# Kernel optimization log

Measured on AMD Instinct MI355X. Metric: run time of the kernel, lower is better.

The kernel has to match this reference:

```python
import jax, jax.numpy as jnp
import numpy as np

# shapes
B, S, D, V = 2, 2048, 1024, 32000
C = 8            # n_cycles
P = 256          # actual planes = min(n_planes_init, D // 2)
EPS = 1.1920929e-07  # torch RMSNorm default eps for float32 (finfo.eps)


def _rmsnorm(x, w):
    ms = jnp.mean(x * x, axis=-1, keepdims=True)
    return x * jax.lax.rsqrt(ms + EPS) * w


def setup_inputs() -> dict:
    key = jax.random.key(0)
    ks = jax.random.split(key, 10)
    tokens = jax.random.randint(ks[0], (B, S), 0, V, dtype=jnp.int32)
    embed_weight = jax.random.normal(ks[1], (V, D), dtype=jnp.float32) * 0.02
    lm_head_weight = jax.random.normal(ks[2], (V, D), dtype=jnp.float32) * 0.02
    out_norm_weight = jnp.ones((D,), dtype=jnp.float32)
    # per-cycle learned params (non-trivial values for numerics)
    angles = jax.random.normal(ks[3], (C, P), dtype=jnp.float32) * 0.1
    scales = 1.0 + jax.random.normal(ks[4], (C, D), dtype=jnp.float32) * 0.01
    shifts = jax.random.normal(ks[5], (C, D), dtype=jnp.float32) * 0.01
    norm_weights = 1.0 + jax.random.normal(ks[6], (C, D), dtype=jnp.float32) * 0.01
    mix_weight = jnp.array([0.1, 0.8, 0.1], dtype=jnp.float32)
    # plane pairs: per-cycle permutation of D, pi = perm[:P], pj = perm[P:2P]
    pi_list, pj_list = [], []
    for c in range(C):
        perm = jax.random.permutation(jax.random.fold_in(ks[7], c), D)
        pi_list.append(perm[:P])
        pj_list.append(perm[P:2 * P])
    pi_all = jnp.stack(pi_list).astype(jnp.int32)  # [C, P]
    pj_all = jnp.stack(pj_list).astype(jnp.int32)  # [C, P]
    return {
        "tokens": tokens,
        "embed_weight": embed_weight,
        "angles": angles,
        "scales": scales,
        "shifts": shifts,
        "norm_weights": norm_weights,
        "mix_weight": mix_weight,
        "out_norm_weight": out_norm_weight,
        "lm_head_weight": lm_head_weight,
        "pi_all": pi_all,
        "pj_all": pj_all,
    }


def reference(tokens, embed_weight, angles, scales, shifts, norm_weights,
              mix_weight, out_norm_weight, lm_head_weight, pi_all, pj_all):
    x = embed_weight[tokens].astype(jnp.float32)  # [B, S, D]
    n_cycles = angles.shape[0]
    for c in range(n_cycles):
        # temporal mix: shifted-left / self / shifted-right
        left = jnp.pad(x[:, :-1, :], ((0, 0), (1, 0), (0, 0)))
        right = jnp.pad(x[:, 1:, :], ((0, 0), (0, 1), (0, 0)))
        x = mix_weight[0] * left + mix_weight[1] * x + mix_weight[2] * right
        # Givens rotations on disjoint plane pairs (gather -> rotate -> scatter)
        pi, pj = pi_all[c], pj_all[c]
        cos_a = jnp.cos(angles[c])
        sin_a = jnp.sin(angles[c])
        xi = x[..., pi]  # [B, S, P]
        xj = x[..., pj]
        x_new = x.at[..., pi].set(xi * cos_a - xj * sin_a)
        x_new = x_new.at[..., pj].set(xi * sin_a + xj * cos_a)
        # scale/shift + SiLU, then RMSNorm residual update
        x_act = jax.nn.silu(x_new * scales[c] + shifts[c])
        x = x + _rmsnorm(x_act - x, norm_weights[c])
    x = _rmsnorm(x, out_norm_weight)
    return jnp.einsum("bsd,vd->bsv", x, lm_head_weight)  # [B, S, V]
```

## Files before the change

kernel.cpp:

```cpp
#include <hip/hip_runtime.h>

#define B_SZ   2
#define S_LEN  2048
#define D_DIM  1024
#define V_DIM  32000
#define NTOK   (B_SZ * S_LEN)
#define NCYC   8
#define NPLANES 256
#define EPS_F  1.1920929e-07f
#define NTILE  2000

typedef float  f32x4  __attribute__((ext_vector_type(4)));
typedef __bf16 bf16x8 __attribute__((ext_vector_type(8)));

__device__ __forceinline__ unsigned short f32_to_bf16(float f) {
    unsigned int u = __builtin_bit_cast(unsigned int, f);
    u += 0x7fffu + ((u >> 16) & 1u);
    return (unsigned short)(u >> 16);
}

__device__ __forceinline__ float4 mix3(float a, const float4& u, float b,
                                       const float4& v, float c, const float4& w) {
    return make_float4(a * u.x + b * v.x + c * w.x,
                       a * u.y + b * v.y + c * w.y,
                       a * u.z + b * v.z + c * w.z,
                       a * u.w + b * v.w + c * w.w);
}

__global__ __launch_bounds__(256) void k_cyc(
    int c,
    const int* __restrict__ tokens, const float* __restrict__ table,
    const float* __restrict__ xin, float* __restrict__ xout,
    const float* __restrict__ angles, const float* __restrict__ scales,
    const float* __restrict__ shifts, const float* __restrict__ normw,
    const float* __restrict__ mixw, const float* __restrict__ outnw,
    unsigned short* __restrict__ xbf,
    const int* __restrict__ pi, const int* __restrict__ pj,
    const float* __restrict__ lmhead, unsigned short* __restrict__ wbf)
{
    __shared__ float lx[4][D_DIM];
    __shared__ float red[4][4];
    const int b = blockIdx.x, tid = threadIdx.x;
    const int wv = tid >> 6, ln = tid & 63;
    const int t0 = b << 2;
    const int s0 = t0 & (S_LEN - 1);

    float4 row[4];
    float4 hl = make_float4(0.f, 0.f, 0.f, 0.f);
    float4 hr = make_float4(0.f, 0.f, 0.f, 0.f);
    if (c == 0) {
        #pragma unroll
        for (int i = 0; i < 4; ++i) {
            const int tok = tokens[t0 + i];
            row[i] = ((const float4*)(table + (size_t)tok * D_DIM))[tid];
        }
        if (s0 > 0) {
            const int tok = tokens[t0 - 1];
            hl = ((const float4*)(table + (size_t)tok * D_DIM))[tid];
        }
        if (s0 + 4 < S_LEN) {
            const int tok = tokens[t0 + 4];
            hr = ((const float4*)(table + (size_t)tok * D_DIM))[tid];
        }
    } else {
        #pragma unroll
        for (int i = 0; i < 4; ++i)
            row[i] = ((const float4*)(xin + (size_t)(t0 + i) * D_DIM))[tid];
        if (s0 > 0)
            hl = ((const float4*)(xin + (size_t)(t0 - 1) * D_DIM))[tid];
        if (s0 + 4 < S_LEN)
            hr = ((const float4*)(xin + (size_t)(t0 + 4) * D_DIM))[tid];
    }
    const float mw0 = mixw[0], mw1 = mixw[1], mw2 = mixw[2];

    float4 m[4];
    m[0] = mix3(mw0, hl,     mw1, row[0], mw2, row[1]);
    m[1] = mix3(mw0, row[0], mw1, row[1], mw2, row[2]);
    m[2] = mix3(mw0, row[1], mw1, row[2], mw2, row[3]);
    m[3] = mix3(mw0, row[2], mw1, row[3], mw2, hr);
    #pragma unroll
    for (int i = 0; i < 4; ++i) ((float4*)lx[i])[tid] = m[i];
    __syncthreads();

    const int ip = pi[tid], jp = pj[tid];
    float sa, ca;
    sincosf(angles[tid], &sa, &ca);
    float xi[4], xj[4];
    #pragma unroll
    for (int i = 0; i < 4; ++i) { xi[i] = lx[i][ip]; xj[i] = lx[i][jp]; }
    #pragma unroll
    for (int i = 0; i < 4; ++i) {
        lx[i][ip] = xi[i] * ca - xj[i] * sa;
        lx[i][jp] = xi[i] * sa + xj[i] * ca;
    }
    __syncthreads();

    const float4 sc = ((const float4*)scales)[tid];
    const float4 sh = ((const float4*)shifts)[tid];
    const float4 nw = ((const float4*)normw)[tid];
    float4 r[4];
    float sum[4];
    #pragma unroll
    for (int i = 0; i < 4; ++i) {
        const float4 xn = ((const float4*)lx[i])[tid];
        const float a0 = xn.x * sc.x + sh.x;
        const float a1 = xn.y * sc.y + sh.y;
        const float a2 = xn.z * sc.z + sh.z;
        const float a3 = xn.w * sc.w + sh.w;
        r[i].x = a0 / (1.f + expf(-a0)) - m[i].x;
        r[i].y = a1 / (1.f + expf(-a1)) - m[i].y;
        r[i].z = a2 / (1.f + expf(-a2)) - m[i].z;
        r[i].w = a3 / (1.f + expf(-a3)) - m[i].w;
        sum[i] = r[i].x * r[i].x + r[i].y * r[i].y
               + r[i].z * r[i].z + r[i].w * r[i].w;
    }
    #pragma unroll
    for (int off = 32; off > 0; off >>= 1)
        #pragma unroll
        for (int i = 0; i < 4; ++i) sum[i] += __shfl_down(sum[i], off, 64);
    if (ln == 0) {
        red[wv][0] = sum[0]; red[wv][1] = sum[1];
        red[wv][2] = sum[2]; red[wv][3] = sum[3];
    }
    __syncthreads();
    #pragma unroll
    for (int i = 0; i < 4; ++i) {
        const float tot = red[0][i] + red[1][i] + red[2][i] + red[3][i];
        const float inv = rsqrtf(tot * (1.0f / D_DIM) + EPS_F);
        row[i].x = m[i].x + r[i].x * inv * nw.x;
        row[i].y = m[i].y + r[i].y * inv * nw.y;
        row[i].z = m[i].z + r[i].z * inv * nw.z;
        row[i].w = m[i].w + r[i].w * inv * nw.w;
    }

    if (c == 7) {
        __syncthreads();
        float fs[4];
        #pragma unroll
        for (int i = 0; i < 4; ++i)
            fs[i] = row[i].x * row[i].x + row[i].y * row[i].y
                  + row[i].z * row[i].z + row[i].w * row[i].w;
        #pragma unroll
        for (int off = 32; off > 0; off >>= 1)
            #pragma unroll
            for (int i = 0; i < 4; ++i) fs[i] += __shfl_down(fs[i], off, 64);
        if (ln == 0) {
            red[wv][0] = fs[0]; red[wv][1] = fs[1];
            red[wv][2] = fs[2]; red[wv][3] = fs[3];
        }
        __syncthreads();
        const float4 w = ((const float4*)outnw)[tid];
        #pragma unroll
        for (int i = 0; i < 4; ++i) {
            const float tot = red[0][i] + red[1][i] + red[2][i] + red[3][i];
            const float inv = rsqrtf(tot * (1.0f / D_DIM) + EPS_F);
            const ushort4 o = make_ushort4(f32_to_bf16(row[i].x * inv * w.x),
                                           f32_to_bf16(row[i].y * inv * w.y),
                                           f32_to_bf16(row[i].z * inv * w.z),
                                           f32_to_bf16(row[i].w * inv * w.w));
            ((ushort4*)xbf)[(size_t)(t0 + i) * 256 + tid] = o;
        }
    } else {
        #pragma unroll
        for (int i = 0; i < 4; ++i)
            ((float4*)(xout + (size_t)(t0 + i) * D_DIM))[tid] = row[i];
    }

    {
        const int end = (c + 1) * 1024000;
        for (int i = c * 1024000 + b * 256 + tid; i < end; i += 262144) {
            const float4 v = ((const float4*)lmhead)[i];
            const ushort4 o = make_ushort4(f32_to_bf16(v.x), f32_to_bf16(v.y),
                                           f32_to_bf16(v.z), f32_to_bf16(v.w));
            ((ushort4*)wbf)[i] = o;
        }
    }
}

#define GLD_LDS(g, l)                                                          \
    __builtin_amdgcn_global_load_lds(                                          \
        (const __attribute__((address_space(1))) void*)(g),                    \
        (__attribute__((address_space(3))) void*)(l), 16, 0, 0)

#define STAGE_A(BUF, H, KT, P) do {                                            \
    GLD_LDS((P) + (size_t)(H) * 131072 + (size_t)(KT) * 64,                    \
            &lds[(BUF) * 32768 + (H) * 8192 + wave * 1024]);                   \
    GLD_LDS((P) + (size_t)(H) * 131072 + 8192 + (size_t)(KT) * 64,             \
            &lds[(BUF) * 32768 + (H) * 8192 + wave * 1024 + 512]);             \
} while (0)

#define STAGE_B(BUF, H, KT, P) do {                                            \
    GLD_LDS((P) + (size_t)(H) * 131072 + (size_t)(KT) * 64,                    \
            &lds[16384 + (BUF) * 32768 + (H) * 8192 + wave * 1024]);           \
    GLD_LDS((P) + (size_t)(H) * 131072 + 8192 + (size_t)(KT) * 64,             \
            &lds[16384 + (BUF) * 32768 + (H) * 8192 + wave * 1024 + 512]);     \
} while (0)

#define RD_A(BUF, MIB) do { _Pragma("unroll")                                  \
    for (int q_ = 0; q_ < 4; ++q_) {                                           \
        afr[q_][0] = *(const bf16x8*)&lds[(BUF) * 32768 + aoff + ((MIB) + q_) * 1024 + kx0]; \
        afr[q_][1] = *(const bf16x8*)&lds[(BUF) * 32768 + aoff + ((MIB) + q_) * 1024 + kx1]; \
    } } while (0)

#define RD_B(BUF, NIB, DST) do { _Pragma("unroll")                             \
    for (int n_ = 0; n_ < 2; ++n_) {                                           \
        DST[n_][0] = *(const bf16x8*)&lds[(BUF) * 32768 + boff + ((NIB) + n_) * 1024 + kx0]; \
        DST[n_][1] = *(const bf16x8*)&lds[(BUF) * 32768 + boff + ((NIB) + n_) * 1024 + kx1]; \
    } } while (0)

#define MFMA16(MIB, NIB, BF) do {                                              \
    __builtin_amdgcn_s_setprio(1);                                             \
    _Pragma("unroll") for (int m_ = 0; m_ < 4; ++m_)                           \
    _Pragma("unroll") for (int n_ = 0; n_ < 2; ++n_) {                         \
        acc[(MIB) + m_][(NIB) + n_] = __builtin_amdgcn_mfma_f32_16x16x32_bf16( \
            afr[m_][0], BF[n_][0], acc[(MIB) + m_][(NIB) + n_], 0, 0, 0);      \
        acc[(MIB) + m_][(NIB) + n_] = __builtin_amdgcn_mfma_f32_16x16x32_bf16( \
            afr[m_][1], BF[n_][1], acc[(MIB) + m_][(NIB) + n_], 0, 0, 0);      \
    }                                                                          \
    __builtin_amdgcn_s_setprio(0); } while (0)

#define PH_SYNC() do { __builtin_amdgcn_s_barrier();                           \
    asm volatile("s_waitcnt lgkmcnt(0)" ::: "memory"); } while (0)
#define PH_END() do { asm volatile("" ::: "memory");                           \
    __builtin_amdgcn_s_barrier(); } while (0)
#define VMCNT4() asm volatile("s_waitcnt vmcnt(4)" ::: "memory")

__global__ __launch_bounds__(512, 2) void k_gemm(
    const unsigned short* __restrict__ A,
    const unsigned short* __restrict__ Bw,
    float* __restrict__ C)
{
    __shared__ __align__(16) unsigned short lds[65536];
    const int tid = threadIdx.x;
    const int wave = tid >> 6, lane = tid & 63;
    const int wm = wave >> 2, wn = wave & 3;
    const int lr = lane & 15, kg = lane >> 4;

    const int xr  = (lane & 7) * 8;
    const int kx0 = (kg * 8) ^ xr;
    const int kx1 = (32 + kg * 8) ^ xr;
    const int aoff = (wm * 128 + lr) * 64;
    const int boff = 16384 + (wn * 64 + lr) * 64;

    const int srow = lane >> 3;
    const int scol = ((lane & 7) ^ srow) * 8;
    const int soff = (wave * 16 + srow) * 1024 + scol;

    const int xcd = blockIdx.x & 7;
    const int rr  = blockIdx.x >> 3;
    const int tbase = xcd * 250 + rr * 8;
    const int ntile_mine = (rr == 31) ? 2 : 8;

    int T  = tbase;
    int bm = T & 15, bn = T >> 4;
    const unsigned short* gA = A  + (size_t)(bm * 256) * 1024 + soff;
    const unsigned short* gB = Bw + (size_t)(bn * 256) * 1024 + soff;

    bf16x8 afr[4][2], b01[2][2], b23[2][2];

    STAGE_A(0, 0, 0, gA); STAGE_A(0, 1, 0, gA);
    STAGE_B(0, 0, 0, gB); STAGE_B(0, 1, 0, gB);
    STAGE_B(1, 0, 1, gB); STAGE_B(1, 1, 1, gB);
    VMCNT4();
    __builtin_amdgcn_s_barrier();

    for (int t = 0; t < ntile_mine; ++t) {
        const bool last = (t == ntile_mine - 1);
        const int Tn = last ? T : T + 1;
        const int bm2 = Tn & 15, bn2 = Tn >> 4;
        const unsigned short* gA2 = A  + (size_t)(bm2 * 256) * 1024 + soff;
        const unsigned short* gB2 = Bw + (size_t)(bn2 * 256) * 1024 + soff;

        f32x4 acc[8][4];
        #pragma unroll
        for (int i = 0; i < 8; ++i)
            #pragma unroll
            for (int j2 = 0; j2 < 4; ++j2) acc[i][j2] = (f32x4){0.f, 0.f, 0.f, 0.f};

        for (int j = 0; j < 8; ++j) {
            const unsigned short* sA = (j == 7) ? gA2 : gA;
            const unsigned short* sB = (j == 7) ? gB2 : gB;
            const int k1 = 2 * j + 1;
            const int k2 = (2 * j + 2) & 15;
            const int k3 = (2 * j + 3) & 15;

            RD_A(0, 0); RD_B(0, 0, b01);
            STAGE_A(1, 0, k1, gA);
            PH_SYNC(); MFMA16(0, 0, b01); PH_END();

            RD_B(0, 2, b23);
            STAGE_A(1, 1, k1, gA);
            PH_SYNC(); MFMA16(0, 2, b23); PH_END();

            RD_A(0, 4);
            STAGE_B(0, 0, k2, sB);
            PH_SYNC(); MFMA16(4, 2, b23); PH_END();

            STAGE_B(0, 1, k2, sB);
            VMCNT4();
            PH_SYNC(); MFMA16(4, 0, b01); PH_END();

            RD_A(1, 0); RD_B(1, 0, b01);
            STAGE_A(0, 0, k2, sA);
            PH_SYNC(); MFMA16(0, 0, b01); PH_END();

            RD_B(1, 2, b23);
            STAGE_A(0, 1, k2, sA);
            PH_SYNC(); MFMA16(0, 2, b23); PH_END();

            RD_A(1, 4);
            STAGE_B(1, 0, k3, sB);
            PH_SYNC(); MFMA16(4, 2, b23); PH_END();

            STAGE_B(1, 1, k3, sB);
            VMCNT4();
            PH_SYNC(); MFMA16(4, 0, b01); PH_END();
        }

        #pragma unroll
        for (int mi = 0; mi < 8; ++mi) {
            const size_t m0 = (size_t)(bm * 256 + wm * 128 + mi * 16 + kg * 4);
            #pragma unroll
            for (int ni = 0; ni < 4; ++ni) {
                const int n = bn * 256 + wn * 64 + ni * 16 + lr;
                float* cp = C + m0 * V_DIM + n;
                cp[0]                 = acc[mi][ni][0];
                cp[(size_t)V_DIM]     = acc[mi][ni][1];
                cp[(size_t)2 * V_DIM] = acc[mi][ni][2];
                cp[(size_t)3 * V_DIM] = acc[mi][ni][3];
            }
        }

        T = Tn; bm = bm2; bn = bn2; gA = gA2; gB = gB2;
    }
}

extern "C" void kernel_launch(void* const* d_in, const int* in_sizes, int n_in,
                              void* d_out, int out_size, void* d_ws, size_t ws_size,
                              hipStream_t stream)
{
    const int*   tokens = (const int*)  d_in[0];
    const float* embedw = (const float*)d_in[1];
    const float* angles = (const float*)d_in[2];
    const float* scales = (const float*)d_in[3];
    const float* shifts = (const float*)d_in[4];
    const float* normw  = (const float*)d_in[5];
    const float* mixw   = (const float*)d_in[6];
    const float* outnw  = (const float*)d_in[7];
    const float* lmhead = (const float*)d_in[8];
    const int*   pi_all = (const int*)  d_in[9];
    const int*   pj_all = (const int*)  d_in[10];
    float* out = (float*)d_out;

    float* xa = (float*)d_ws;
    float* xb = xa + (size_t)NTOK * D_DIM;
    unsigned short* xbf = (unsigned short*)(xb + (size_t)NTOK * D_DIM);
    unsigned short* wbf = xbf + (size_t)NTOK * D_DIM;

    for (int c = 0; c < NCYC; ++c) {
        const float* xin = (c & 1) ? xb : xa;
        float* xout = (c & 1) ? xa : xb;
        k_cyc<<<NTOK / 4, 256, 0, stream>>>(c, tokens, embedw, xin, xout,
            angles + c * NPLANES, scales + c * D_DIM, shifts + c * D_DIM,
            normw + c * D_DIM, mixw, outnw, xbf,
            pi_all + c * NPLANES, pj_all + c * NPLANES, lmhead, wbf);
    }

    k_gemm<<<256, 512, 0, stream>>>(xbf, wbf, out);
}
```

Measured before the change: 423.1 us.

## Fuse all eight cycles into one kernel with halo recompute in LDS

```diff
diff --git a/kernel.cpp b/kernel.cpp
--- a/kernel.cpp
+++ b/kernel.cpp
@@ -19,161 +19,137 @@
     return (unsigned short)(u >> 16);
 }
 
-__device__ __forceinline__ float4 mix3(float a, const float4& u, float b,
-                                       const float4& v, float c, const float4& w) {
-    return make_float4(a * u.x + b * v.x + c * w.x,
-                       a * u.y + b * v.y + c * w.y,
-                       a * u.z + b * v.z + c * w.z,
-                       a * u.w + b * v.w + c * w.w);
-}
-
-__global__ __launch_bounds__(256) void k_cyc(
-    int c,
+__global__ __launch_bounds__(512, 2) void k_chain(
     const int* __restrict__ tokens, const float* __restrict__ table,
-    const float* __restrict__ xin, float* __restrict__ xout,
     const float* __restrict__ angles, const float* __restrict__ scales,
     const float* __restrict__ shifts, const float* __restrict__ normw,
     const float* __restrict__ mixw, const float* __restrict__ outnw,
-    unsigned short* __restrict__ xbf,
-    const int* __restrict__ pi, const int* __restrict__ pj,
-    const float* __restrict__ lmhead, unsigned short* __restrict__ wbf)
+    const int* __restrict__ pi_all, const int* __restrict__ pj_all,
+    const float* __restrict__ lmhead,
+    unsigned short* __restrict__ xbf, unsigned short* __restrict__ wbf)
 {
-    __shared__ float lx[4][D_DIM];
-    __shared__ float red[4][4];
-    const int b = blockIdx.x, tid = threadIdx.x;
+    __shared__ float lx[32][D_DIM];
+    __shared__ float red[8][32];
+    const int blk = blockIdx.x, tid = threadIdx.x;
     const int wv = tid >> 6, ln = tid & 63;
-    const int t0 = b << 2;
+    const int t0 = blk << 4;
     const int s0 = t0 & (S_LEN - 1);
-
-    float4 row[4];
-    float4 hl = make_float4(0.f, 0.f, 0.f, 0.f);
-    float4 hr = make_float4(0.f, 0.f, 0.f, 0.f);
-    if (c == 0) {
-        #pragma unroll
-        for (int i = 0; i < 4; ++i) {
-            const int tok = tokens[t0 + i];
-            row[i] = ((const float4*)(table + (size_t)tok * D_DIM))[tid];
-        }
-        if (s0 > 0) {
-            const int tok = tokens[t0 - 1];
-            hl = ((const float4*)(table + (size_t)tok * D_DIM))[tid];
-        }
-        if (s0 + 4 < S_LEN) {
-            const int tok = tokens[t0 + 4];
-            hr = ((const float4*)(table + (size_t)tok * D_DIM))[tid];
-        }
-    } else {
-        #pragma unroll
-        for (int i = 0; i < 4; ++i)
-            row[i] = ((const float4*)(xin + (size_t)(t0 + i) * D_DIM))[tid];
-        if (s0 > 0)
-            hl = ((const float4*)(xin + (size_t)(t0 - 1) * D_DIM))[tid];
-        if (s0 + 4 < S_LEN)
-            hr = ((const float4*)(xin + (size_t)(t0 + 4) * D_DIM))[tid];
-    }
+    const int seqbase = t0 & ~(S_LEN - 1);
+    const int c2 = tid << 1;
+
     const float mw0 = mixw[0], mw1 = mixw[1], mw2 = mixw[2];
 
-    float4 m[4];
-    m[0] = mix3(mw0, hl,     mw1, row[0], mw2, row[1]);
-    m[1] = mix3(mw0, row[0], mw1, row[1], mw2, row[2]);
-    m[2] = mix3(mw0, row[1], mw1, row[2], mw2, row[3]);
-    m[3] = mix3(mw0, row[2], mw1, row[3], mw2, hr);
+    unsigned int svmask = 0;
     #pragma unroll
-    for (int i = 0; i < 4; ++i) ((float4*)lx[i])[tid] = m[i];
+    for (int r = 0; r < 32; ++r) {
+        const int s = s0 - 8 + r;
+        const bool sv = (s >= 0) && (s < S_LEN);
+        if (sv) svmask |= (1u << r);
+        float2 v = make_float2(0.f, 0.f);
+        if (sv) {
+            const int tok = tokens[seqbase + s];
+            v = *(const float2*)(table + (size_t)tok * D_DIM + c2);
+        }
+        lx[r][c2] = v.x; lx[r][c2 + 1] = v.y;
+    }
     __syncthreads();
 
-    const int ip = pi[tid], jp = pj[tid];
-    float sa, ca;
-    sincosf(angles[tid], &sa, &ca);
-    float xi[4], xj[4];
+    float2 mreg[31], rres[31];
+
+    for (int c = 0; c < NCYC; ++c) {
+        const float2 sc = *(const float2*)(scales + c * D_DIM + c2);
+        const float2 sh = *(const float2*)(shifts + c * D_DIM + c2);
+        const float2 nw = *(const float2*)(normw  + c * D_DIM + c2);
+        const int p    = tid & 255;
+        const int half = tid >> 8;
+        const int ip = pi_all[c * NPLANES + p];
+        const int jp = pj_all[c * NPLANES + p];
+        float sa, ca;
+        sincosf(angles[c * NPLANES + p], &sa, &ca);
+
+        #pragma unroll
+        for (int r = 1; r <= 30; ++r) {
+            if (r >= c + 1 && r < 31 - c && ((svmask >> r) & 1)) {
+                const float2 a = make_float2(lx[r - 1][c2], lx[r - 1][c2 + 1]);
+                const float2 b = make_float2(lx[r][c2],     lx[r][c2 + 1]);
+                const float2 d = make_float2(lx[r + 1][c2], lx[r + 1][c2 + 1]);
+                mreg[r].x = mw0 * a.x + mw1 * b.x + mw2 * d.x;
+                mreg[r].y = mw0 * a.y + mw1 * b.y + mw2 * d.y;
+            }
+        }
+        __syncthreads();
+        #pragma unroll
+        for (int r = 1; r <= 30; ++r) {
+            if (r >= c + 1 && r < 31 - c && ((svmask >> r) & 1)) {
+                lx[r][c2] = mreg[r].x; lx[r][c2 + 1] = mreg[r].y;
+            }
+        }
+        __syncthreads();
+        #pragma unroll
+        for (int r = 1; r <= 30; ++r) {
+            if (r >= c + 1 && r < 31 - c && ((svmask >> r) & 1) && (r & 1) == half) {
+                const float xi = lx[r][ip], xj = lx[r][jp];
+                lx[r][ip] = xi * ca - xj * sa;
+                lx[r][jp] = xi * sa + xj * ca;
+            }
+        }
+        __syncthreads();
+        #pragma unroll
+        for (int r = 1; r <= 30; ++r) {
+            if (r >= c + 1 && r < 31 - c && ((svmask >> r) & 1)) {
+                const float v0 = lx[r][c2], v1 = lx[r][c2 + 1];
+                const float a0 = v0 * sc.x + sh.x;
+                const float a1 = v1 * sc.y + sh.y;
+                rres[r].x = a0 / (1.f + expf(-a0)) - mreg[r].x;
+                rres[r].y = a1 / (1.f + expf(-a1)) - mreg[r].y;
+                float pp = rres[r].x * rres[r].x + rres[r].y * rres[r].y;
+                #pragma unroll
+                for (int off = 32; off > 0; off >>= 1)
+                    pp += __shfl_down(pp, off, 64);
+                if (ln == 0) red[wv][r] = pp;
+            }
+        }
+        __syncthreads();
+        #pragma unroll
+        for (int r = 1; r <= 30; ++r) {
+            if (r >= c + 1 && r < 31 - c && ((svmask >> r) & 1)) {
+                const float tot = red[0][r] + red[1][r] + red[2][r] + red[3][r]
+                                + red[4][r] + red[5][r] + red[6][r] + red[7][r];
+                const float inv = rsqrtf(tot * (1.0f / D_DIM) + EPS_F);
+                lx[r][c2]     = mreg[r].x + rres[r].x * inv * nw.x;
+                lx[r][c2 + 1] = mreg[r].y + rres[r].y * inv * nw.y;
+            }
+        }
+        __syncthreads();
+    }
+
+    const float2 ow = *(const float2*)(outnw + c2);
     #pragma unroll
-    for (int i = 0; i < 4; ++i) { xi[i] = lx[i][ip]; xj[i] = lx[i][jp]; }
-    #pragma unroll
-    for (int i = 0; i < 4; ++i) {
-        lx[i][ip] = xi[i] * ca - xj[i] * sa;
-        lx[i][jp] = xi[i] * sa + xj[i] * ca;
-    }
-    __syncthreads();
-
-    const float4 sc = ((const float4*)scales)[tid];
-    const float4 sh = ((const float4*)shifts)[tid];
-    const float4 nw = ((const float4*)normw)[tid];
-    float4 r[4];
-    float sum[4];
-    #pragma unroll
-    for (int i = 0; i < 4; ++i) {
-        const float4 xn = ((const float4*)lx[i])[tid];
-        const float a0 = xn.x * sc.x + sh.x;
-        const float a1 = xn.y * sc.y + sh.y;
-        const float a2 = xn.z * sc.z + sh.z;
-        const float a3 = xn.w * sc.w + sh.w;
-        r[i].x = a0 / (1.f + expf(-a0)) - m[i].x;
-        r[i].y = a1 / (1.f + expf(-a1)) - m[i].y;
-        r[i].z = a2 / (1.f + expf(-a2)) - m[i].z;
-        r[i].w = a3 / (1.f + expf(-a3)) - m[i].w;
-        sum[i] = r[i].x * r[i].x + r[i].y * r[i].y
-               + r[i].z * r[i].z + r[i].w * r[i].w;
-    }
-    #pragma unroll
-    for (int off = 32; off > 0; off >>= 1)
-        #pragma unroll
-        for (int i = 0; i < 4; ++i) sum[i] += __shfl_down(sum[i], off, 64);
-    if (ln == 0) {
-        red[wv][0] = sum[0]; red[wv][1] = sum[1];
-        red[wv][2] = sum[2]; red[wv][3] = sum[3];
+    for (int r = 8; r < 24; ++r) {
+        const float v0 = lx[r][c2], v1 = lx[r][c2 + 1];
+        float pp = v0 * v0 + v1 * v1;
+        #pragma unroll
+        for (int off = 32; off > 0; off >>= 1)
+            pp += __shfl_down(pp, off, 64);
+        if (ln == 0) red[wv][r - 8] = pp;
     }
     __syncthreads();
     #pragma unroll
-    for (int i = 0; i < 4; ++i) {
-        const float tot = red[0][i] + red[1][i] + red[2][i] + red[3][i];
+    for (int r = 8; r < 24; ++r) {
+        const float tot = red[0][r - 8] + red[1][r - 8] + red[2][r - 8] + red[3][r - 8]
+                        + red[4][r - 8] + red[5][r - 8] + red[6][r - 8] + red[7][r - 8];
         const float inv = rsqrtf(tot * (1.0f / D_DIM) + EPS_F);
-        row[i].x = m[i].x + r[i].x * inv * nw.x;
-        row[i].y = m[i].y + r[i].y * inv * nw.y;
-        row[i].z = m[i].z + r[i].z * inv * nw.z;
-        row[i].w = m[i].w + r[i].w * inv * nw.w;
-    }
-
-    if (c == 7) {
-        __syncthreads();
-        float fs[4];
-        #pragma unroll
-        for (int i = 0; i < 4; ++i)
-            fs[i] = row[i].x * row[i].x + row[i].y * row[i].y
-                  + row[i].z * row[i].z + row[i].w * row[i].w;
-        #pragma unroll
-        for (int off = 32; off > 0; off >>= 1)
-            #pragma unroll
-            for (int i = 0; i < 4; ++i) fs[i] += __shfl_down(fs[i], off, 64);
-        if (ln == 0) {
-            red[wv][0] = fs[0]; red[wv][1] = fs[1];
-            red[wv][2] = fs[2]; red[wv][3] = fs[3];
-        }
-        __syncthreads();
-        const float4 w = ((const float4*)outnw)[tid];
-        #pragma unroll
-        for (int i = 0; i < 4; ++i) {
-            const float tot = red[0][i] + red[1][i] + red[2][i] + red[3][i];
-            const float inv = rsqrtf(tot * (1.0f / D_DIM) + EPS_F);
-            const ushort4 o = make_ushort4(f32_to_bf16(row[i].x * inv * w.x),
-                                           f32_to_bf16(row[i].y * inv * w.y),
-                                           f32_to_bf16(row[i].z * inv * w.z),
-                                           f32_to_bf16(row[i].w * inv * w.w));
-            ((ushort4*)xbf)[(size_t)(t0 + i) * 256 + tid] = o;
-        }
-    } else {
-        #pragma unroll
-        for (int i = 0; i < 4; ++i)
-            ((float4*)(xout + (size_t)(t0 + i) * D_DIM))[tid] = row[i];
-    }
-
-    {
-        const int end = (c + 1) * 1024000;
-        for (int i = c * 1024000 + b * 256 + tid; i < end; i += 262144) {
-            const float4 v = ((const float4*)lmhead)[i];
-            const ushort4 o = make_ushort4(f32_to_bf16(v.x), f32_to_bf16(v.y),
-                                           f32_to_bf16(v.z), f32_to_bf16(v.w));
-            ((ushort4*)wbf)[i] = o;
-        }
+        const float v0 = lx[r][c2], v1 = lx[r][c2 + 1];
+        ushort2 o = make_ushort2(f32_to_bf16(v0 * inv * ow.x),
+                                 f32_to_bf16(v1 * inv * ow.y));
+        *(ushort2*)(xbf + (size_t)(t0 + r - 8) * D_DIM + c2) = o;
+    }
+
+    for (int i = blk * 512 + tid; i < (V_DIM * D_DIM) / 4; i += 256 * 512) {
+        const float4 v = ((const float4*)lmhead)[i];
+        const ushort4 o = make_ushort4(f32_to_bf16(v.x), f32_to_bf16(v.y),
+                                       f32_to_bf16(v.z), f32_to_bf16(v.w));
+        ((ushort4*)wbf)[i] = o;
     }
 }
 
@@ -352,19 +328,11 @@
     const int*   pj_all = (const int*)  d_in[10];
     float* out = (float*)d_out;
 
-    float* xa = (float*)d_ws;
-    float* xb = xa + (size_t)NTOK * D_DIM;
-    unsigned short* xbf = (unsigned short*)(xb + (size_t)NTOK * D_DIM);
+    unsigned short* xbf = (unsigned short*)d_ws;
     unsigned short* wbf = xbf + (size_t)NTOK * D_DIM;
 
-    for (int c = 0; c < NCYC; ++c) {
-        const float* xin = (c & 1) ? xb : xa;
-        float* xout = (c & 1) ? xa : xb;
-        k_cyc<<<NTOK / 4, 256, 0, stream>>>(c, tokens, embedw, xin, xout,
-            angles + c * NPLANES, scales + c * D_DIM, shifts + c * D_DIM,
-            normw + c * D_DIM, mixw, outnw, xbf,
-            pi_all + c * NPLANES, pj_all + c * NPLANES, lmhead, wbf);
-    }
+    k_chain<<<NTOK / 16, 512, 0, stream>>>(tokens, embedw, angles, scales,
+        shifts, normw, mixw, outnw, pi_all, pj_all, lmhead, xbf, wbf);
 
     k_gemm<<<256, 512, 0, stream>>>(xbf, wbf, out);
 }
```

After: 467.9 us. 1.11x slower.
